# Kernel optimization log

Measured on AMD Instinct MI355X. Metric: run time of the kernel, lower is better.

Reference implementation:

```python
import jax, jax.numpy as jnp
import numpy as np

D = 512
FF = 1024
B = 512


def _ln(x, g, b):
    mu = x.mean(-1, keepdims=True)
    var = ((x - mu) ** 2).mean(-1, keepdims=True)
    return (x - mu) / jnp.sqrt(var + 1e-5) * g + b


def _mha(x, kpm, wqkv, bqkv, wo, bo, h):
    # torch nn.MultiheadAttention with key_padding_mask (True = pad)
    Bx, L, d = x.shape
    dh = d // h
    qkv = x @ wqkv.T + bqkv                      # [B,L,3D]
    q, k, v = jnp.split(qkv, 3, axis=-1)
    q = q.reshape(Bx, L, h, dh).transpose(0, 2, 1, 3)
    k = k.reshape(Bx, L, h, dh).transpose(0, 2, 1, 3)
    v = v.reshape(Bx, L, h, dh).transpose(0, 2, 1, 3)
    s = jnp.einsum('bhqd,bhkd->bhqk', q, k) * (1.0 / float(np.sqrt(dh)))
    s = jnp.where(kpm[:, None, None, :], -jnp.inf, s)
    a = jax.nn.softmax(s, axis=-1)
    o = jnp.einsum('bhqk,bhkd->bhqd', a, v).transpose(0, 2, 1, 3).reshape(Bx, L, d)
    return o @ wo.T + bo


def _enc(x, kpm, p, h):
    # torch TransformerEncoderLayer, post-norm, relu, eval mode (no dropout)
    wqkv, bqkv, wo, bo, g1, be1, w1, b1, w2, b2, g2, be2 = p
    x = _ln(x + _mha(x, kpm, wqkv, bqkv, wo, bo, h), g1, be1)
    x = _ln(x + jax.nn.relu(x @ w1.T + b1) @ w2.T + b2, g2, be2)
    return x


def _split_padding(x, nums):
    # flat [N,D] -> padded [B,L,D] + padding mask (True = pad); nums is concrete np
    nums = np.asarray(nums)
    Bx = nums.shape[0]
    L = int(nums.max())
    start = np.concatenate([[0], np.cumsum(nums)])[:-1]
    idx = np.clip(start[:, None] + np.arange(L)[None, :], 0, x.shape[0] - 1)
    valid = np.arange(L)[None, :] < nums[:, None]
    padded = jnp.where(jnp.asarray(valid)[..., None], x[jnp.asarray(idx)], 0.0)
    return padded, jnp.asarray(~valid)


def _lengths():
    node_nums = 64 + (np.arange(B) % 65)                 # total 48924
    ring_counts = 4 + (np.arange(B) % 5)                 # total 3069
    R = int(ring_counts.sum())
    ring_sizes = 5 + (np.arange(R) % 4)                  # total 19947
    return node_nums, ring_counts, ring_sizes


def _make_enc_params(key, scale=0.05):
    ks = jax.random.split(key, 4)
    return (
        jax.random.normal(ks[0], (3 * D, D), jnp.float32) * scale,
        jnp.zeros((3 * D,), jnp.float32),
        jax.random.normal(ks[1], (D, D), jnp.float32) * scale,
        jnp.zeros((D,), jnp.float32),
        jnp.ones((D,), jnp.float32), jnp.zeros((D,), jnp.float32),
        jax.random.normal(ks[2], (FF, D), jnp.float32) * scale,
        jnp.zeros((FF,), jnp.float32),
        jax.random.normal(ks[3], (D, FF), jnp.float32) * scale,
        jnp.zeros((D,), jnp.float32),
        jnp.ones((D,), jnp.float32), jnp.zeros((D,), jnp.float32),
    )


def setup_inputs() -> dict:
    key = jax.random.key(0)
    k_x, k_idx, k_tok, k_r, k_m = jax.random.split(key, 5)
    node_nums, ring_counts, ring_sizes = _lengths()
    ptr = np.concatenate([[0], np.cumsum(node_nums)]).astype(np.int64)
    N = int(ptr[-1])
    M = int(ring_sizes.sum())
    inp = {
        'x': jax.random.normal(k_x, (N, D), jnp.float32),
        'ptr': jnp.asarray(ptr),
        'rings_node_index': jax.random.randint(k_idx, (M,), 0, N),
        'rings_node_nums': jnp.asarray(ring_sizes.astype(np.int64)),
        'mol_rings_nums': jnp.asarray(ring_counts.astype(np.int64)),
    }
    kc, kr2, ke = jax.random.split(k_tok, 3)
    inp['CLS'] = jax.random.normal(kc, (1, D), jnp.float32)
    inp['RING'] = jax.random.normal(kr2, (1, D), jnp.float32)
    inp['END'] = jax.random.normal(ke, (1, D), jnp.float32)
    rp = _make_enc_params(k_r)
    mp = _make_enc_params(k_m)
    rnames = ['r_wqkv', 'r_bqkv', 'r_wo', 'r_bo', 'r_ln1g', 'r_ln1b', 'r_w1', 'r_b1', 'r_w2', 'r_b2', 'r_ln2g', 'r_ln2b']
    mnames = ['m_wqkv', 'm_bqkv', 'm_wo', 'm_bo', 'm_ln1g', 'm_ln1b', 'm_w1', 'm_b1', 'm_w2', 'm_b2', 'm_ln2g', 'm_ln2b']
    inp.update(dict(zip(rnames, rp)))
    inp.update(dict(zip(mnames, mp)))
    return inp


def _forward(x, CLS, RING, END, rp, mp, ptr, rni, rnn, mrn):
    ptr = np.asarray(ptr)
    rnn = np.asarray(rnn)
    mrn = np.asarray(mrn)
    node_nums = ptr[1:] - ptr[:-1]
    # nodes padding
    X, X_mask = _split_padding(x, node_nums)             # [B,Ln,D]
    # rings attention
    xr = x[rni]                                          # [M,D]
    Xr_pad, r_pm = _split_padding(xr, rnn)               # [R,Lr,D]
    Xe = _enc(Xr_pad, r_pm, rp, 2)
    amax = jnp.argmax(jnp.abs(Xe), axis=1)               # [R,D]
    rings_vec = jnp.take_along_axis(Xe, amax[:, None, :], axis=1)[:, 0]  # [R,D]
    Xr, Xr_mask = _split_padding(rings_vec, mrn)         # [B,Lrm,D]
    # assemble [CLS, X, RING, Xr, END]
    Bx = X.shape[0]
    seq = jnp.concatenate([
        jnp.broadcast_to(CLS, (Bx, 1, D)), X,
        jnp.broadcast_to(RING, (Bx, 1, D)), Xr,
        jnp.broadcast_to(END, (Bx, 1, D))], axis=1)
    z = jnp.zeros((Bx, 1), bool)
    kpm = jnp.concatenate([z, X_mask, z, Xr_mask, z], axis=1)
    seq = _enc(seq, kpm, mp, 4)
    mol_vec = seq[:, 0]
    # ragged extraction of node / ring vectors
    Ln = int(node_nums.max())
    Lrm = int(mrn.max())
    node_block = seq[:, 1:Ln + 1].reshape(Bx * Ln, D)
    nvalid = (np.arange(Ln)[None, :] < node_nums[:, None]).ravel()
    node_vec = node_block[jnp.asarray(np.nonzero(nvalid)[0])]
    ring_block = seq[:, -Lrm - 1:-1].reshape(Bx * Lrm, D)
    rvalid = (np.arange(Lrm)[None, :] < mrn[:, None]).ravel()
    ring_vec = ring_block[jnp.asarray(np.nonzero(rvalid)[0])]
    return mol_vec, node_vec, ring_vec


def reference(x, ptr, rings_node_index, rings_node_nums, mol_rings_nums,
              CLS, RING, END,
              r_wqkv, r_bqkv, r_wo, r_bo, r_ln1g, r_ln1b, r_w1, r_b1, r_w2, r_b2, r_ln2g, r_ln2b,
              m_wqkv, m_bqkv, m_wo, m_bo, m_ln1g, m_ln1b, m_w1, m_b1, m_w2, m_b2, m_ln2g, m_ln2b):
    rp = (r_wqkv, r_bqkv, r_wo, r_bo, r_ln1g, r_ln1b, r_w1, r_b1, r_w2, r_b2, r_ln2g, r_ln2b)
    mp = (m_wqkv, m_bqkv, m_wo, m_bo, m_ln1g, m_ln1b, m_w1, m_b1, m_w2, m_b2, m_ln2g, m_ln2b)
    return _forward(x, CLS, RING, END, rp, mp, ptr, rings_node_index, rings_node_nums, mol_rings_nums)
```

## Files before the change

### kernel.cpp

```cpp
#include <hip/hip_runtime.h>
#include <math.h>

#define D_ 512
#define LSEQ 139
#define LRING 8
#define LDK 40

typedef __bf16 bf16x8 __attribute__((ext_vector_type(8)));
typedef float f32x4 __attribute__((ext_vector_type(4)));

__device__ __forceinline__ void f2split(float f, unsigned short& h, unsigned short& l) {
    unsigned int u = __float_as_uint(f);
    h = (unsigned short)(u >> 16);
    float r = f - __uint_as_float(u & 0xFFFF0000u);
    l = (unsigned short)(__float_as_uint(r) >> 16);
}

__global__ void scan_kernel(const int* __restrict__ rnn, int R,
                            const int* __restrict__ mrn, int Bm,
                            int* __restrict__ rs, int* __restrict__ ms) {
    __shared__ int lds[256];
    int tid = threadIdx.x;
    int chunk = (R + 255) / 256;
    int sum = 0;
    for (int i = 0; i < chunk; ++i) {
        int idx = tid * chunk + i;
        if (idx < R) sum += rnn[idx];
    }
    lds[tid] = sum;
    __syncthreads();
    if (tid == 0) {
        int run = 0;
        for (int t = 0; t < 256; ++t) { int tmp = lds[t]; lds[t] = run; run += tmp; }
    }
    __syncthreads();
    int off = lds[tid];
    for (int i = 0; i < chunk; ++i) {
        int idx = tid * chunk + i;
        if (idx < R) { rs[idx] = off; off += rnn[idx]; }
    }
    __syncthreads();
    chunk = (Bm + 255) / 256;
    sum = 0;
    for (int i = 0; i < chunk; ++i) {
        int idx = tid * chunk + i;
        if (idx < Bm) sum += mrn[idx];
    }
    __syncthreads();
    lds[tid] = sum;
    __syncthreads();
    if (tid == 0) {
        int run = 0;
        for (int t = 0; t < 256; ++t) { int tmp = lds[t]; lds[t] = run; run += tmp; }
    }
    __syncthreads();
    off = lds[tid];
    for (int i = 0; i < chunk; ++i) {
        int idx = tid * chunk + i;
        if (idx < Bm) { ms[idx] = off; off += mrn[idx]; }
    }
}

__global__ void convert_w(const float* __restrict__ src, unsigned short* __restrict__ dst, int n4) {
    int t = blockIdx.x * blockDim.x + threadIdx.x;
    if (t >= n4) return;
    const float4 v = *(const float4*)(src + (size_t)t * 4);
    unsigned int u0 = __float_as_uint(v.x), u1 = __float_as_uint(v.y),
                 u2 = __float_as_uint(v.z), u3 = __float_as_uint(v.w);
    u0 = (u0 + 0x7FFFu + ((u0 >> 16) & 1)) >> 16;
    u1 = (u1 + 0x7FFFu + ((u1 >> 16) & 1)) >> 16;
    u2 = (u2 + 0x7FFFu + ((u2 >> 16) & 1)) >> 16;
    u3 = (u3 + 0x7FFFu + ((u3 >> 16) & 1)) >> 16;
    *(uint2*)(dst + (size_t)t * 4) = make_uint2(u0 | (u1 << 16), u2 | (u3 << 16));
}

__global__ void build_xr(const float* __restrict__ x, const int* __restrict__ rni,
                         const int* __restrict__ rnn, const int* __restrict__ rs,
                         float* __restrict__ out, int rBase, int RC) {
    int t = blockIdx.x * blockDim.x + threadIdx.x;
    int total = RC * LRING * (D_ / 4);
    if (t >= total) return;
    int c4 = (t & 127) * 4;
    int row = t >> 7;
    int rl = row >> 3, l = row & 7;
    int r = rBase + rl;
    float4 v = make_float4(0.f, 0.f, 0.f, 0.f);
    if (l < rnn[r]) {
        int node = rni[rs[r] + l];
        v = *(const float4*)(x + (size_t)node * D_ + c4);
    }
    *(float4*)(out + (size_t)row * D_ + c4) = v;
}

template <bool RELU, bool RES>
__global__ __launch_bounds__(256) void gemm_nt(const float* __restrict__ A,
                                               const float* __restrict__ Bw,
                                               const float* __restrict__ bias,
                                               const float* Res, float* C,
                                               int M, int N, int K) {
    __shared__ __align__(16) float As[16][132];
    __shared__ __align__(16) float Bs[16][132];
    const int bm = blockIdx.y * 128, bn = blockIdx.x * 128;
    const int tid = threadIdx.x;
    const int ty = tid >> 4, tx = tid & 15;
    const int sr = tid >> 1;
    const int sc = (tid & 1) * 8;
    float acc[8][8];
#pragma unroll
    for (int i = 0; i < 8; ++i)
#pragma unroll
        for (int j = 0; j < 8; ++j) acc[i][j] = 0.f;
    const float4 z4 = make_float4(0.f, 0.f, 0.f, 0.f);
    const int arow = bm + sr;
    const bool aok = arow < M;
    for (int k0 = 0; k0 < K; k0 += 16) {
        float4 av0 = z4, av1 = z4;
        if (aok) {
            av0 = *(const float4*)(A + (size_t)arow * K + k0 + sc);
            av1 = *(const float4*)(A + (size_t)arow * K + k0 + sc + 4);
        }
        const float4 bv0 = *(const float4*)(Bw + (size_t)(bn + sr) * K + k0 + sc);
        const float4 bv1 = *(const float4*)(Bw + (size_t)(bn + sr) * K + k0 + sc + 4);
        __syncthreads();
        As[sc + 0][sr] = av0.x; As[sc + 1][sr] = av0.y; As[sc + 2][sr] = av0.z; As[sc + 3][sr] = av0.w;
        As[sc + 4][sr] = av1.x; As[sc + 5][sr] = av1.y; As[sc + 6][sr] = av1.z; As[sc + 7][sr] = av1.w;
        Bs[sc + 0][sr] = bv0.x; Bs[sc + 1][sr] = bv0.y; Bs[sc + 2][sr] = bv0.z; Bs[sc + 3][sr] = bv0.w;
        Bs[sc + 4][sr] = bv1.x; Bs[sc + 5][sr] = bv1.y; Bs[sc + 6][sr] = bv1.z; Bs[sc + 7][sr] = bv1.w;
        __syncthreads();
#pragma unroll
        for (int k = 0; k < 16; ++k) {
            float a[8], b[8];
            *(float4*)&a[0] = *(const float4*)&As[k][ty * 8];
            *(float4*)&a[4] = *(const float4*)&As[k][ty * 8 + 4];
            *(float4*)&b[0] = *(const float4*)&Bs[k][tx * 8];
            *(float4*)&b[4] = *(const float4*)&Bs[k][tx * 8 + 4];
#pragma unroll
            for (int i = 0; i < 8; ++i)
#pragma unroll
                for (int j = 0; j < 8; ++j) acc[i][j] += a[i] * b[j];
        }
    }
    const int n = bn + tx * 8;
    float bvv[8];
    *(float4*)&bvv[0] = *(const float4*)(bias + n);
    *(float4*)&bvv[4] = *(const float4*)(bias + n + 4);
#pragma unroll
    for (int i = 0; i < 8; ++i) {
        int m = bm + ty * 8 + i;
        if (m >= M) continue;
        float r[8];
#pragma unroll
        for (int j = 0; j < 8; ++j) r[j] = acc[i][j] + bvv[j];
        if (RES) {
            float rv[8];
            *(float4*)&rv[0] = *(const float4*)(Res + (size_t)m * N + n);
            *(float4*)&rv[4] = *(const float4*)(Res + (size_t)m * N + n + 4);
#pragma unroll
            for (int j = 0; j < 8; ++j) r[j] += rv[j];
        }
        if (RELU) {
#pragma unroll
            for (int j = 0; j < 8; ++j) r[j] = fmaxf(r[j], 0.f);
        }
        *(float4*)(C + (size_t)m * N + n) = make_float4(r[0], r[1], r[2], r[3]);
        *(float4*)(C + (size_t)m * N + n + 4) = make_float4(r[4], r[5], r[6], r[7]);
    }
}

template <bool RELU, bool RES, bool OSPLIT>
__global__ __launch_bounds__(256, 2) void gemm_bf16(
        const unsigned short* __restrict__ Ah, const unsigned short* __restrict__ Al,
        const unsigned short* __restrict__ Bw, const float* __restrict__ bias,
        const float* __restrict__ Res, float* __restrict__ C,
        unsigned short* __restrict__ Oh, unsigned short* __restrict__ Ol,
        int M, int N, int K) {
    __shared__ __align__(16) unsigned short sAh[128][LDK];
    __shared__ __align__(16) unsigned short sAl[128][LDK];
    __shared__ __align__(16) unsigned short sB[128][LDK];
    const int bm = blockIdx.y * 128, bn = blockIdx.x * 128;
    const int tid = threadIdx.x;
    const int lane = tid & 63, wid = tid >> 6;
    const int wr = wid >> 1, wc = wid & 1;
    const int fr = lane & 15, fq = lane >> 4;
    const int sr = tid >> 2;
    const int sc = (tid & 3) * 8;
    f32x4 acc[4][4];
#pragma unroll
    for (int m = 0; m < 4; ++m)
#pragma unroll
        for (int n = 0; n < 4; ++n) {
            acc[m][n][0] = 0.f; acc[m][n][1] = 0.f;
            acc[m][n][2] = 0.f; acc[m][n][3] = 0.f;
        }
    const int r0 = bm + sr, r1 = r0 + 64;
    const bool ok0 = r0 < M, ok1 = r1 < M;
    for (int k0 = 0; k0 < K; k0 += 32) {
        uint4 a0 = make_uint4(0, 0, 0, 0), a1 = a0, al0 = a0, al1 = a0;
        if (ok0) {
            a0  = *(const uint4*)(Ah + (size_t)r0 * K + k0 + sc);
            al0 = *(const uint4*)(Al + (size_t)r0 * K + k0 + sc);
        }
        if (ok1) {
            a1  = *(const uint4*)(Ah + (size_t)r1 * K + k0 + sc);
            al1 = *(const uint4*)(Al + (size_t)r1 * K + k0 + sc);
        }
        const uint4 b0 = *(const uint4*)(Bw + (size_t)(bn + sr) * K + k0 + sc);
        const uint4 b1 = *(const uint4*)(Bw + (size_t)(bn + sr + 64) * K + k0 + sc);
        __syncthreads();
        *(uint4*)&sAh[sr][sc] = a0;  *(uint4*)&sAh[sr + 64][sc] = a1;
        *(uint4*)&sAl[sr][sc] = al0; *(uint4*)&sAl[sr + 64][sc] = al1;
        *(uint4*)&sB[sr][sc]  = b0;  *(uint4*)&sB[sr + 64][sc]  = b1;
        __syncthreads();
        bf16x8 bfr[4];
#pragma unroll
        for (int n = 0; n < 4; ++n)
            bfr[n] = *(const bf16x8*)&sB[wc * 64 + n * 16 + fr][fq * 8];
#pragma unroll
        for (int m = 0; m < 4; ++m) {
            bf16x8 ah = *(const bf16x8*)&sAh[wr * 64 + m * 16 + fr][fq * 8];
            bf16x8 al = *(const bf16x8*)&sAl[wr * 64 + m * 16 + fr][fq * 8];
#pragma unroll
            for (int n = 0; n < 4; ++n)
                acc[m][n] = __builtin_amdgcn_mfma_f32_16x16x32_bf16(ah, bfr[n], acc[m][n], 0, 0, 0);
#pragma unroll
            for (int n = 0; n < 4; ++n)
                acc[m][n] = __builtin_amdgcn_mfma_f32_16x16x32_bf16(al, bfr[n], acc[m][n], 0, 0, 0);
        }
    }
    float bv[4];
#pragma unroll
    for (int n = 0; n < 4; ++n) bv[n] = bias[bn + wc * 64 + n * 16 + fr];
#pragma unroll
    for (int m = 0; m < 4; ++m) {
#pragma unroll
        for (int i = 0; i < 4; ++i) {
            int row = bm + wr * 64 + m * 16 + fq * 4 + i;
            if (row >= M) continue;
#pragma unroll
            for (int n = 0; n < 4; ++n) {
                int col = bn + wc * 64 + n * 16 + fr;
                float v = acc[m][n][i] + bv[n];
                if (RES) v += Res[(size_t)row * N + col];
                if (RELU) v = fmaxf(v, 0.f);
                if (OSPLIT) {
                    unsigned short h, l;
                    f2split(v, h, l);
                    Oh[(size_t)row * N + col] = h;
                    Ol[(size_t)row * N + col] = l;
                } else {
                    C[(size_t)row * N + col] = v;
                }
            }
        }
    }
}

__global__ __launch_bounds__(256) void ring_attn(const float* __restrict__ qkv,
                                                 const int* __restrict__ rnn,
                                                 float* __restrict__ ctx, int rBase) {
    __shared__ float qs[8][260], ks[8][260], vs[8][260];
    __shared__ float sS[8][8];
    __shared__ float pS[8][8];
    const int hh = blockIdx.x;
    const int rl = blockIdx.y;
    const int tid = threadIdx.x;
    const int rn = rnn[rBase + rl];
    const float* base = qkv + (size_t)rl * 8 * 1536;
    for (int i = tid; i < 8 * 256; i += 256) {
        int l = i >> 8, c = i & 255;
        const float* p = base + (size_t)l * 1536 + hh * 256 + c;
        qs[l][c] = p[0];
        ks[l][c] = p[512];
        vs[l][c] = p[1024];
    }
    __syncthreads();
    if (tid < 64) {
        int i = tid >> 3, j = tid & 7;
        float s = -30000.f;
        if (j < rn) {
            float d = 0.f;
            for (int c = 0; c < 256; ++c) d += qs[i][c] * ks[j][c];
            s = d * 0.0625f;
        }
        sS[i][j] = s;
    }
    __syncthreads();
    if (tid < 8) {
        int i = tid;
        float mx = -30000.f;
#pragma unroll
        for (int j = 0; j < 8; ++j) mx = fmaxf(mx, sS[i][j]);
        float p[8], sum = 0.f;
#pragma unroll
        for (int j = 0; j < 8; ++j) { p[j] = __expf(sS[i][j] - mx); sum += p[j]; }
        float inv = 1.f / sum;
#pragma unroll
        for (int j = 0; j < 8; ++j) pS[i][j] = p[j] * inv;
    }
    __syncthreads();
    {
        int d = tid;
#pragma unroll
        for (int i = 0; i < 8; ++i) {
            float a = 0.f;
#pragma unroll
            for (int j = 0; j < 8; ++j) a += pS[i][j] * vs[j][d];
            ctx[(size_t)(rl * 8 + i) * 512 + hh * 256 + d] = a;
        }
    }
}

__global__ void argmax_pick(const float* __restrict__ Xe, float* __restrict__ rv, int RC) {
    int t = blockIdx.x * blockDim.x + threadIdx.x;
    if (t >= RC * 512) return;
    int r = t >> 9, d = t & 511;
    const float* p = Xe + (size_t)r * 8 * 512 + d;
    float best = fabsf(p[0]);
    int pos = 0;
#pragma unroll
    for (int l = 1; l < 8; ++l) {
        float v = fabsf(p[(size_t)l * 512]);
        if (v > best) { best = v; pos = l; }
    }
    rv[t] = p[(size_t)pos * 512];
}

__global__ void build_seq(const float* __restrict__ x, const float* __restrict__ rv,
                          const float* __restrict__ CLS, const float* __restrict__ RING,
                          const float* __restrict__ END, const int* __restrict__ ptr,
                          const int* __restrict__ mrn, const int* __restrict__ ms,
                          float* __restrict__ seq, unsigned short* __restrict__ oh,
                          unsigned short* __restrict__ ol, int bBase, int CB) {
    int t = blockIdx.x * blockDim.x + threadIdx.x;
    int total = CB * LSEQ * 128;
    if (t >= total) return;
    int c4 = (t & 127) * 4;
    int row = t >> 7;
    int bl = row / LSEQ, p = row - bl * LSEQ;
    int b = bBase + bl;
    const float* src = nullptr;
    if (p == 0) src = CLS;
    else if (p <= 128) {
        int i = p - 1;
        int nn = ptr[b + 1] - ptr[b];
        if (i < nn) src = x + (size_t)(ptr[b] + i) * 512;
    } else if (p == 129) src = RING;
    else if (p <= 137) {
        int i = p - 130;
        if (i < mrn[b]) src = rv + (size_t)(ms[b] + i) * 512;
    } else src = END;
    float4 v = src ? *(const float4*)(src + c4) : make_float4(0.f, 0.f, 0.f, 0.f);
    *(float4*)(seq + (size_t)row * 512 + c4) = v;
    unsigned short h0, h1, h2, h3, l0, l1, l2, l3;
    f2split(v.x, h0, l0); f2split(v.y, h1, l1);
    f2split(v.z, h2, l2); f2split(v.w, h3, l3);
    *(uint2*)(oh + (size_t)row * 512 + c4) = make_uint2(h0 | (h1 << 16), h2 | (h3 << 16));
    *(uint2*)(ol + (size_t)row * 512 + c4) = make_uint2(l0 | (l1 << 16), l2 | (l3 << 16));
}

__device__ __forceinline__ bool key_valid_mol(int j, int nn, int nr) {
    if (j == 0 || j == 129 || j == 138) return true;
    if (j <= 128) return (j - 1) < nn;
    if (j <= 137) return (j - 130) < nr;
    return false;
}

__global__ __launch_bounds__(256) void mol_attn(const float* __restrict__ qkv,
                                                const int* __restrict__ ptr,
                                                const int* __restrict__ mrn,
                                                unsigned short* __restrict__ ctxh,
                                                unsigned short* __restrict__ ctxl,
                                                int bBase) {
    __shared__ __align__(16) float qs[16][132];
    __shared__ __align__(16) float ks[32][132];
    __shared__ __align__(16) float vs[32][132];
    __shared__ float st[16][33];
    const int qt = blockIdx.x, hh = blockIdx.y, bl = blockIdx.z;
    const int b = bBase + bl;
    const int tid = threadIdx.x;
    const int qi = tid >> 4, dj = tid & 15;
    const int nn = ptr[b + 1] - ptr[b];
    const int nr = mrn[b];
    const int q0 = qt * 16;
    const float* base = qkv + (size_t)bl * LSEQ * 1536;
    {
        int qrow = q0 + qi;
        float4 v0 = make_float4(0.f, 0.f, 0.f, 0.f), v1 = v0;
        if (qrow < LSEQ) {
            const float* p = base + (size_t)qrow * 1536 + hh * 128 + dj * 8;
            v0 = *(const float4*)p;
            v1 = *(const float4*)(p + 4);
        }
        *(float4*)&qs[qi][dj * 8] = v0;
        *(float4*)&qs[qi][dj * 8 + 4] = v1;
    }
    float m_i = -30000.f, l_i = 0.f;
    float acc[8] = {0.f, 0.f, 0.f, 0.f, 0.f, 0.f, 0.f, 0.f};
    for (int j0 = 0; j0 < LSEQ; j0 += 32) {
        __syncthreads();
        {
            int jl = tid >> 3;
            int jr = j0 + jl;
            int c = (tid & 7) * 16;
            float4 kk[4], vv[4];
            if (jr < LSEQ) {
                const float* pk = base + (size_t)jr * 1536 + 512 + hh * 128 + c;
#pragma unroll
                for (int q = 0; q < 4; ++q) {
                    kk[q] = *(const float4*)(pk + q * 4);
                    vv[q] = *(const float4*)(pk + 512 + q * 4);
                }
            } else {
#pragma unroll
                for (int q = 0; q < 4; ++q) { kk[q] = make_float4(0.f, 0.f, 0.f, 0.f); vv[q] = kk[q]; }
            }
#pragma unroll
            for (int q = 0; q < 4; ++q) {
                *(float4*)&ks[jl][c + q * 4] = kk[q];
                *(float4*)&vs[jl][c + q * 4] = vv[q];
            }
        }
        __syncthreads();
#pragma unroll
        for (int t2 = 0; t2 < 2; ++t2) {
            int jj = dj + t2 * 16;
            int j = j0 + jj;
            float s = -30000.f;
            if (j < LSEQ && key_valid_mol(j, nn, nr)) {
                float d = 0.f;
#pragma unroll
                for (int c = 0; c < 128; c += 4) {
                    float4 a = *(const float4*)&qs[qi][c];
                    float4 kk = *(const float4*)&ks[jj][c];
                    d += a.x * kk.x + a.y * kk.y + a.z * kk.z + a.w * kk.w;
                }
                s = d * 0.08838834764831845f;
            }
            st[qi][jj] = s;
        }
        __syncthreads();
        float cmax = -30000.f;
#pragma unroll
        for (int j = 0; j < 32; ++j) cmax = fmaxf(cmax, st[qi][j]);
        float m_new = fmaxf(m_i, cmax);
        float alpha = __expf(m_i - m_new);
        l_i *= alpha;
#pragma unroll
        for (int d = 0; d < 8; ++d) acc[d] *= alpha;
        for (int j = 0; j < 32; ++j) {
            float pj = __expf(st[qi][j] - m_new);
            l_i += pj;
            float4 v0 = *(const float4*)&vs[j][dj * 8];
            float4 v1 = *(const float4*)&vs[j][dj * 8 + 4];
            acc[0] += pj * v0.x; acc[1] += pj * v0.y; acc[2] += pj * v0.z; acc[3] += pj * v0.w;
            acc[4] += pj * v1.x; acc[5] += pj * v1.y; acc[6] += pj * v1.z; acc[7] += pj * v1.w;
        }
        m_i = m_new;
    }
    int qrow = q0 + qi;
    if (qrow < LSEQ) {
        float inv = 1.f / l_i;
        size_t o = (size_t)(bl * LSEQ + qrow) * 512 + hh * 128 + dj * 8;
        unsigned int hw[4], lw[4];
#pragma unroll
        for (int i2 = 0; i2 < 4; ++i2) {
            unsigned short ha, hb, la, lb;
            f2split(acc[2 * i2] * inv, ha, la);
            f2split(acc[2 * i2 + 1] * inv, hb, lb);
            hw[i2] = (unsigned int)ha | ((unsigned int)hb << 16);
            lw[i2] = (unsigned int)la | ((unsigned int)lb << 16);
        }
        *(uint4*)(ctxh + o) = make_uint4(hw[0], hw[1], hw[2], hw[3]);
        *(uint4*)(ctxl + o) = make_uint4(lw[0], lw[1], lw[2], lw[3]);
    }
}

__global__ __launch_bounds__(64) void ln_kernel(float* X, const float* __restrict__ gam,
                                                const float* __restrict__ bet,
                                                unsigned short* __restrict__ oh,
                                                unsigned short* __restrict__ ol) {
    const size_t row = blockIdx.x;
    const int tid = threadIdx.x;
    float* p = X + row * 512 + tid * 8;
    float4 v0 = *(float4*)p, v1 = *(float4*)(p + 4);
    float s = v0.x + v0.y + v0.z + v0.w + v1.x + v1.y + v1.z + v1.w;
#pragma unroll
    for (int off = 32; off; off >>= 1) s += __shfl_xor(s, off, 64);
    float mu = s * (1.f / 512.f);
    float d[8] = {v0.x - mu, v0.y - mu, v0.z - mu, v0.w - mu,
                  v1.x - mu, v1.y - mu, v1.z - mu, v1.w - mu};
    float s2 = 0.f;
#pragma unroll
    for (int i = 0; i < 8; ++i) s2 += d[i] * d[i];
#pragma unroll
    for (int off = 32; off; off >>= 1) s2 += __shfl_xor(s2, off, 64);
    float inv = 1.f / sqrtf(s2 * (1.f / 512.f) + 1e-5f);
    const float* gp = gam + tid * 8;
    const float* bp = bet + tid * 8;
    float4 g0 = *(const float4*)gp, g1 = *(const float4*)(gp + 4);
    float4 b0 = *(const float4*)bp, b1 = *(const float4*)(bp + 4);
    float y[8];
    y[0] = d[0] * inv * g0.x + b0.x; y[1] = d[1] * inv * g0.y + b0.y;
    y[2] = d[2] * inv * g0.z + b0.z; y[3] = d[3] * inv * g0.w + b0.w;
    y[4] = d[4] * inv * g1.x + b1.x; y[5] = d[5] * inv * g1.y + b1.y;
    y[6] = d[6] * inv * g1.z + b1.z; y[7] = d[7] * inv * g1.w + b1.w;
    *(float4*)p = make_float4(y[0], y[1], y[2], y[3]);
    *(float4*)(p + 4) = make_float4(y[4], y[5], y[6], y[7]);
    if (oh) {
        unsigned int hw[4], lw[4];
#pragma unroll
        for (int i2 = 0; i2 < 4; ++i2) {
            unsigned short ha, hb, la, lb;
            f2split(y[2 * i2], ha, la);
            f2split(y[2 * i2 + 1], hb, lb);
            hw[i2] = (unsigned int)ha | ((unsigned int)hb << 16);
            lw[i2] = (unsigned int)la | ((unsigned int)lb << 16);
        }
        size_t o = row * 512 + tid * 8;
        *(uint4*)(oh + o) = make_uint4(hw[0], hw[1], hw[2], hw[3]);
        *(uint4*)(ol + o) = make_uint4(lw[0], lw[1], lw[2], lw[3]);
    }
}

__global__ void scatter_out(const float* __restrict__ seq, const int* __restrict__ ptr,
                            const int* __restrict__ mrn, const int* __restrict__ ms,
                            float* __restrict__ out_mol, float* __restrict__ out_node,
                            float* __restrict__ out_ring, int bBase, int CB) {
    int t = blockIdx.x * blockDim.x + threadIdx.x;
    int total = CB * LSEQ * 128;
    if (t >= total) return;
    int c4 = (t & 127) * 4;
    int row = t >> 7;
    int bl = row / LSEQ, p = row - bl * LSEQ;
    int b = bBase + bl;
    float4 v = *(const float4*)(seq + (size_t)row * 512 + c4);
    if (p == 0) {
        *(float4*)(out_mol + (size_t)b * 512 + c4) = v;
    } else if (p <= 128) {
        int i = p - 1;
        int nn = ptr[b + 1] - ptr[b];
        if (i < nn) *(float4*)(out_node + (size_t)(ptr[b] + i) * 512 + c4) = v;
    } else if (p >= 130 && p <= 137) {
        int i = p - 130;
        if (i < mrn[b]) *(float4*)(out_ring + (size_t)(ms[b] + i) * 512 + c4) = v;
    }
}

extern "C" void kernel_launch(void* const* d_in, const int* in_sizes, int n_in,
                              void* d_out, int out_size, void* d_ws, size_t ws_size,
                              hipStream_t stream) {
    const float* x      = (const float*)d_in[0];
    const int*   ptr    = (const int*)d_in[1];
    const int*   rni    = (const int*)d_in[2];
    const int*   rnn    = (const int*)d_in[3];
    const int*   mrn    = (const int*)d_in[4];
    const float* CLS    = (const float*)d_in[5];
    const float* RINGt  = (const float*)d_in[6];
    const float* ENDt   = (const float*)d_in[7];
    const float* r_wqkv = (const float*)d_in[8];
    const float* r_bqkv = (const float*)d_in[9];
    const float* r_wo   = (const float*)d_in[10];
    const float* r_bo   = (const float*)d_in[11];
    const float* r_ln1g = (const float*)d_in[12];
    const float* r_ln1b = (const float*)d_in[13];
    const float* r_w1   = (const float*)d_in[14];
    const float* r_b1   = (const float*)d_in[15];
    const float* r_w2   = (const float*)d_in[16];
    const float* r_b2   = (const float*)d_in[17];
    const float* r_ln2g = (const float*)d_in[18];
    const float* r_ln2b = (const float*)d_in[19];
    const float* m_wqkv = (const float*)d_in[20];
    const float* m_bqkv = (const float*)d_in[21];
    const float* m_wo   = (const float*)d_in[22];
    const float* m_bo   = (const float*)d_in[23];
    const float* m_ln1g = (const float*)d_in[24];
    const float* m_ln1b = (const float*)d_in[25];
    const float* m_w1   = (const float*)d_in[26];
    const float* m_b1   = (const float*)d_in[27];
    const float* m_w2   = (const float*)d_in[28];
    const float* m_b2   = (const float*)d_in[29];
    const float* m_ln2g = (const float*)d_in[30];
    const float* m_ln2b = (const float*)d_in[31];

    const int N  = in_sizes[0] / D_;
    const int R  = in_sizes[3];
    const int Bm = in_sizes[4];

    char* w = (char*)d_ws;
    size_t off = 0;
    float* rings_vec = (float*)(w + off); off += (size_t)R * 512 * 4;
    int* rs = (int*)(w + off); off += (size_t)R * 4;
    int* ms = (int*)(w + off); off += (size_t)Bm * 4;
    off = (off + 255) & ~(size_t)255;
    unsigned short* b_m_wqkv = (unsigned short*)(w + off);
    unsigned short* b_m_wo   = b_m_wqkv + 1536 * 512;
    unsigned short* b_m_w1   = b_m_wo   + 512 * 512;
    unsigned short* b_m_w2   = b_m_w1   + 1024 * 512;
    off += (size_t)(1536 * 512 + 512 * 512 + 1024 * 512 + 512 * 1024) * 2;
    off = (off + 255) & ~(size_t)255;

    size_t avail = (ws_size > off) ? (ws_size - off) : 0;
    const size_t perMolA = (size_t)LSEQ * 512 * 4;
    const size_t perMolQ = (size_t)LSEQ * 1536 * 4;
    const size_t perMolP = (size_t)LSEQ * 512 * 2;
    const size_t perMol  = perMolA + perMolQ + 2 * perMolP;
    int molChunk = (int)(avail / perMol);
    if (molChunk > Bm) molChunk = Bm;
    if (molChunk < 1) return;
    int ringChunk = molChunk * 17;
    if (ringChunk > R) ringChunk = R;
    float* bufA = (float*)(w + off); off += (size_t)molChunk * perMolA;
    float* bufQ = (float*)(w + off); off += (size_t)molChunk * perMolQ;
    unsigned short* P0h = (unsigned short*)(w + off);
    unsigned short* P0l = P0h + (size_t)molChunk * LSEQ * 512;
    float* bufC = (float*)P0h;
    unsigned short* P1h = (unsigned short*)bufQ;
    unsigned short* P1l = P1h + (size_t)molChunk * LSEQ * 1024;

    float* out_mol  = (float*)d_out;
    float* out_node = out_mol + (size_t)Bm * 512;
    float* out_ring = out_node + (size_t)N * 512;

    scan_kernel<<<1, 256, 0, stream>>>(rnn, R, mrn, Bm, rs, ms);

    convert_w<<<(1536 * 512 / 4 + 255) / 256, 256, 0, stream>>>(m_wqkv, b_m_wqkv, 1536 * 512 / 4);
    convert_w<<<(512 * 512 / 4 + 255) / 256, 256, 0, stream>>>(m_wo, b_m_wo, 512 * 512 / 4);
    convert_w<<<(1024 * 512 / 4 + 255) / 256, 256, 0, stream>>>(m_w1, b_m_w1, 1024 * 512 / 4);
    convert_w<<<(512 * 1024 / 4 + 255) / 256, 256, 0, stream>>>(m_w2, b_m_w2, 512 * 1024 / 4);

    for (int r0 = 0; r0 < R; r0 += ringChunk) {
        int RC = (R - r0 < ringChunk) ? (R - r0) : ringChunk;
        int TrC = RC * LRING;
        build_xr<<<(TrC * 128 + 255) / 256, 256, 0, stream>>>(x, rni, rnn, rs, bufA, r0, RC);
        gemm_nt<false, false><<<dim3(1536 / 128, (TrC + 127) / 128), 256, 0, stream>>>(
            bufA, r_wqkv, r_bqkv, nullptr, bufQ, TrC, 1536, 512);
        ring_attn<<<dim3(2, RC), 256, 0, stream>>>(bufQ, rnn, bufC, r0);
        gemm_nt<false, true><<<dim3(512 / 128, (TrC + 127) / 128), 256, 0, stream>>>(
            bufC, r_wo, r_bo, bufA, bufA, TrC, 512, 512);
        ln_kernel<<<TrC, 64, 0, stream>>>(bufA, r_ln1g, r_ln1b, nullptr, nullptr);
        gemm_nt<true, false><<<dim3(1024 / 128, (TrC + 127) / 128), 256, 0, stream>>>(
            bufA, r_w1, r_b1, nullptr, bufQ, TrC, 1024, 512);
        gemm_nt<false, true><<<dim3(512 / 128, (TrC + 127) / 128), 256, 0, stream>>>(
            bufQ, r_w2, r_b2, bufA, bufA, TrC, 512, 1024);
        ln_kernel<<<TrC, 64, 0, stream>>>(bufA, r_ln2g, r_ln2b, nullptr, nullptr);
        argmax_pick<<<(RC * 512 + 255) / 256, 256, 0, stream>>>(bufA, rings_vec + (size_t)r0 * 512, RC);
    }

    for (int c0 = 0; c0 < Bm; c0 += molChunk) {
        int CB = (Bm - c0 < molChunk) ? (Bm - c0) : molChunk;
        int TmC = CB * LSEQ;
        build_seq<<<(TmC * 128 + 255) / 256, 256, 0, stream>>>(
            x, rings_vec, CLS, RINGt, ENDt, ptr, mrn, ms, bufA, P0h, P0l, c0, CB);
        gemm_bf16<false, false, false><<<dim3(1536 / 128, (TmC + 127) / 128), 256, 0, stream>>>(
            P0h, P0l, b_m_wqkv, m_bqkv, nullptr, bufQ, nullptr, nullptr, TmC, 1536, 512);
        mol_attn<<<dim3((LSEQ + 15) / 16, 4, CB), 256, 0, stream>>>(bufQ, ptr, mrn, P0h, P0l, c0);
        gemm_bf16<false, true, false><<<dim3(512 / 128, (TmC + 127) / 128), 256, 0, stream>>>(
            P0h, P0l, b_m_wo, m_bo, bufA, bufA, nullptr, nullptr, TmC, 512, 512);
        ln_kernel<<<TmC, 64, 0, stream>>>(bufA, m_ln1g, m_ln1b, P0h, P0l);
        gemm_bf16<true, false, true><<<dim3(1024 / 128, (TmC + 127) / 128), 256, 0, stream>>>(
            P0h, P0l, b_m_w1, m_b1, nullptr, nullptr, P1h, P1l, TmC, 1024, 512);
        gemm_bf16<false, true, false><<<dim3(512 / 128, (TmC + 127) / 128), 256, 0, stream>>>(
            P1h, P1l, b_m_w2, m_b2, bufA, bufA, nullptr, nullptr, TmC, 512, 1024);
        ln_kernel<<<TmC, 64, 0, stream>>>(bufA, m_ln2g, m_ln2b, nullptr, nullptr);
        scatter_out<<<(TmC * 128 + 255) / 256, 256, 0, stream>>>(
            bufA, ptr, mrn, ms, out_mol, out_node, out_ring, c0, CB);
    }
}
```

Measured before the change: 3.590 ms.

## Load full K/V head slice into LDS once per block, loop over query tiles

The mol attention kernel now launches one block per (head, molecule) instead of per (query tile, head, molecule). Each block stages all 139 K and V rows of its head into shared memory once, then iterates over all query tiles, so the K/V global reloads across query tiles go away. In exchange, LDS use grows to about 150KB per block, which limits occupancy to one block per CU, and the grid shrinks by a factor of 9, reducing parallelism.

```diff
diff --git a/kernel.cpp b/kernel.cpp
--- a/kernel.cpp
+++ b/kernel.cpp
@@ -372,106 +372,98 @@
                                                 unsigned short* __restrict__ ctxl,
                                                 int bBase) {
     __shared__ __align__(16) float qs[16][132];
-    __shared__ __align__(16) float ks[32][132];
-    __shared__ __align__(16) float vs[32][132];
+    __shared__ __align__(16) float ks[LSEQ][132];
+    __shared__ __align__(16) float vs[LSEQ][132];
     __shared__ float st[16][33];
-    const int qt = blockIdx.x, hh = blockIdx.y, bl = blockIdx.z;
+    const int hh = blockIdx.x, bl = blockIdx.y;
     const int b = bBase + bl;
     const int tid = threadIdx.x;
     const int qi = tid >> 4, dj = tid & 15;
     const int nn = ptr[b + 1] - ptr[b];
     const int nr = mrn[b];
-    const int q0 = qt * 16;
     const float* base = qkv + (size_t)bl * LSEQ * 1536;
-    {
-        int qrow = q0 + qi;
-        float4 v0 = make_float4(0.f, 0.f, 0.f, 0.f), v1 = v0;
-        if (qrow < LSEQ) {
-            const float* p = base + (size_t)qrow * 1536 + hh * 128 + dj * 8;
-            v0 = *(const float4*)p;
-            v1 = *(const float4*)(p + 4);
-        }
-        *(float4*)&qs[qi][dj * 8] = v0;
-        *(float4*)&qs[qi][dj * 8 + 4] = v1;
-    }
-    float m_i = -30000.f, l_i = 0.f;
-    float acc[8] = {0.f, 0.f, 0.f, 0.f, 0.f, 0.f, 0.f, 0.f};
-    for (int j0 = 0; j0 < LSEQ; j0 += 32) {
+    for (int i = tid; i < LSEQ * 32; i += 256) {
+        int row = i >> 5, cq = (i & 31) * 4;
+        const float* pk = base + (size_t)row * 1536 + 512 + hh * 128 + cq;
+        float4 kk = *(const float4*)pk;
+        float4 vv = *(const float4*)(pk + 512);
+        *(float4*)&ks[row][cq] = kk;
+        *(float4*)&vs[row][cq] = vv;
+    }
+    __syncthreads();
+    for (int qt = 0; qt < (LSEQ + 15) / 16; ++qt) {
+        const int q0 = qt * 16;
         __syncthreads();
         {
-            int jl = tid >> 3;
-            int jr = j0 + jl;
-            int c = (tid & 7) * 16;
-            float4 kk[4], vv[4];
-            if (jr < LSEQ) {
-                const float* pk = base + (size_t)jr * 1536 + 512 + hh * 128 + c;
-#pragma unroll
-                for (int q = 0; q < 4; ++q) {
-                    kk[q] = *(const float4*)(pk + q * 4);
-                    vv[q] = *(const float4*)(pk + 512 + q * 4);
+            int qrow = q0 + qi;
+            float4 v0 = make_float4(0.f, 0.f, 0.f, 0.f), v1 = v0;
+            if (qrow < LSEQ) {
+                const float* p = base + (size_t)qrow * 1536 + hh * 128 + dj * 8;
+                v0 = *(const float4*)p;
+                v1 = *(const float4*)(p + 4);
+            }
+            *(float4*)&qs[qi][dj * 8] = v0;
+            *(float4*)&qs[qi][dj * 8 + 4] = v1;
+        }
+        __syncthreads();
+        float m_i = -30000.f, l_i = 0.f;
+        float acc[8] = {0.f, 0.f, 0.f, 0.f, 0.f, 0.f, 0.f, 0.f};
+        for (int j0 = 0; j0 < LSEQ; j0 += 32) {
+#pragma unroll
+            for (int t2 = 0; t2 < 2; ++t2) {
+                int jj = dj + t2 * 16;
+                int j = j0 + jj;
+                float s = -30000.f;
+                if (j < LSEQ && key_valid_mol(j, nn, nr)) {
+                    float d = 0.f;
+#pragma unroll
+                    for (int c = 0; c < 128; c += 4) {
+                        float4 a = *(const float4*)&qs[qi][c];
+                        float4 kk = *(const float4*)&ks[j][c];
+                        d += a.x * kk.x + a.y * kk.y + a.z * kk.z + a.w * kk.w;
+                    }
+                    s = d * 0.08838834764831845f;
                 }
-            } else {
-#pragma unroll
-                for (int q = 0; q < 4; ++q) { kk[q] = make_float4(0.f, 0.f, 0.f, 0.f); vv[q] = kk[q]; }
+                st[qi][jj] = s;
             }
-#pragma unroll
-            for (int q = 0; q < 4; ++q) {
-                *(float4*)&ks[jl][c + q * 4] = kk[q];
-                *(float4*)&vs[jl][c + q * 4] = vv[q];
+            __syncthreads();
+            float cmax = -30000.f;
+#pragma unroll
+            for (int j = 0; j < 32; ++j) cmax = fmaxf(cmax, st[qi][j]);
+            float m_new = fmaxf(m_i, cmax);
+            float alpha = __expf(m_i - m_new);
+            l_i *= alpha;
+#pragma unroll
+            for (int d = 0; d < 8; ++d) acc[d] *= alpha;
+            for (int j = 0; j < 32; ++j) {
+                float pj = __expf(st[qi][j] - m_new);
+                l_i += pj;
+                int jg = j0 + j;
+                int jv = (jg < LSEQ) ? jg : (LSEQ - 1);
+                float4 v0 = *(const float4*)&vs[jv][dj * 8];
+                float4 v1 = *(const float4*)&vs[jv][dj * 8 + 4];
+                acc[0] += pj * v0.x; acc[1] += pj * v0.y; acc[2] += pj * v0.z; acc[3] += pj * v0.w;
+                acc[4] += pj * v1.x; acc[5] += pj * v1.y; acc[6] += pj * v1.z; acc[7] += pj * v1.w;
             }
-        }
-        __syncthreads();
-#pragma unroll
-        for (int t2 = 0; t2 < 2; ++t2) {
-            int jj = dj + t2 * 16;
-            int j = j0 + jj;
-            float s = -30000.f;
-            if (j < LSEQ && key_valid_mol(j, nn, nr)) {
-                float d = 0.f;
-#pragma unroll
-                for (int c = 0; c < 128; c += 4) {
-                    float4 a = *(const float4*)&qs[qi][c];
-                    float4 kk = *(const float4*)&ks[jj][c];
-                    d += a.x * kk.x + a.y * kk.y + a.z * kk.z + a.w * kk.w;
-                }
-                s = d * 0.08838834764831845f;
+            m_i = m_new;
+            __syncthreads();
+        }
+        int qrow = q0 + qi;
+        if (qrow < LSEQ) {
+            float inv = 1.f / l_i;
+            size_t o = (size_t)(bl * LSEQ + qrow) * 512 + hh * 128 + dj * 8;
+            unsigned int hw[4], lw[4];
+#pragma unroll
+            for (int i2 = 0; i2 < 4; ++i2) {
+                unsigned short ha, hb, la, lb;
+                f2split(acc[2 * i2] * inv, ha, la);
+                f2split(acc[2 * i2 + 1] * inv, hb, lb);
+                hw[i2] = (unsigned int)ha | ((unsigned int)hb << 16);
+                lw[i2] = (unsigned int)la | ((unsigned int)lb << 16);
             }
-            st[qi][jj] = s;
-        }
-        __syncthreads();
-        float cmax = -30000.f;
-#pragma unroll
-        for (int j = 0; j < 32; ++j) cmax = fmaxf(cmax, st[qi][j]);
-        float m_new = fmaxf(m_i, cmax);
-        float alpha = __expf(m_i - m_new);
-        l_i *= alpha;
-#pragma unroll
-        for (int d = 0; d < 8; ++d) acc[d] *= alpha;
-        for (int j = 0; j < 32; ++j) {
-            float pj = __expf(st[qi][j] - m_new);
-            l_i += pj;
-            float4 v0 = *(const float4*)&vs[j][dj * 8];
-            float4 v1 = *(const float4*)&vs[j][dj * 8 + 4];
-            acc[0] += pj * v0.x; acc[1] += pj * v0.y; acc[2] += pj * v0.z; acc[3] += pj * v0.w;
-            acc[4] += pj * v1.x; acc[5] += pj * v1.y; acc[6] += pj * v1.z; acc[7] += pj * v1.w;
-        }
-        m_i = m_new;
-    }
-    int qrow = q0 + qi;
-    if (qrow < LSEQ) {
-        float inv = 1.f / l_i;
-        size_t o = (size_t)(bl * LSEQ + qrow) * 512 + hh * 128 + dj * 8;
-        unsigned int hw[4], lw[4];
-#pragma unroll
-        for (int i2 = 0; i2 < 4; ++i2) {
-            unsigned short ha, hb, la, lb;
-            f2split(acc[2 * i2] * inv, ha, la);
-            f2split(acc[2 * i2 + 1] * inv, hb, lb);
-            hw[i2] = (unsigned int)ha | ((unsigned int)hb << 16);
-            lw[i2] = (unsigned int)la | ((unsigned int)lb << 16);
-        }
-        *(uint4*)(ctxh + o) = make_uint4(hw[0], hw[1], hw[2], hw[3]);
-        *(uint4*)(ctxl + o) = make_uint4(lw[0], lw[1], lw[2], lw[3]);
+            *(uint4*)(ctxh + o) = make_uint4(hw[0], hw[1], hw[2], hw[3]);
+            *(uint4*)(ctxl + o) = make_uint4(lw[0], lw[1], lw[2], lw[3]);
+        }
     }
 }
 
@@ -653,7 +645,7 @@
             x, rings_vec, CLS, RINGt, ENDt, ptr, mrn, ms, bufA, P0h, P0l, c0, CB);
         gemm_bf16<false, false, false><<<dim3(1536 / 128, (TmC + 127) / 128), 256, 0, stream>>>(
             P0h, P0l, b_m_wqkv, m_bqkv, nullptr, bufQ, nullptr, nullptr, TmC, 1536, 512);
-        mol_attn<<<dim3((LSEQ + 15) / 16, 4, CB), 256, 0, stream>>>(bufQ, ptr, mrn, P0h, P0l, c0);
+        mol_attn<<<dim3(4, CB), 256, 0, stream>>>(bufQ, ptr, mrn, P0h, P0l, c0);
         gemm_bf16<false, true, false><<<dim3(512 / 128, (TmC + 127) / 128), 256, 0, stream>>>(
             P0h, P0l, b_m_wo, m_bo, bufA, bufA, nullptr, nullptr, TmC, 512, 512);
         ln_kernel<<<TmC, 64, 0, stream>>>(bufA, m_ln1g, m_ln1b, P0h, P0l);
```

Result: slower. 4.395 ms (+22.4%).
